# Optimization experiments

Hardware: AMD Instinct MI355X
Metric: run time of the kernel (lower is better)

The kernel has to match this reference:

```python
import jax, jax.numpy as jnp
import numpy as np

B, N, D = 8, 1024, 512
H = 8
DH = D // H
EPS_DIST = 1e-8
EPS_LN = 1e-5


def _layer_norm(x, gamma, beta):
    mu = jnp.mean(x, axis=-1, keepdims=True)
    var = jnp.mean((x - mu) ** 2, axis=-1, keepdims=True)
    return (x - mu) * jax.lax.rsqrt(var + EPS_LN) * gamma + beta


def setup_inputs() -> dict:
    key = jax.random.key(0)
    ks = jax.random.split(key, 6)
    scale = 1.0 / np.sqrt(D)
    inp = {
        "x": jax.random.normal(ks[0], (B, N, D), dtype=jnp.float32),
        "Wq": jax.random.normal(ks[1], (D, D), dtype=jnp.float32) * scale,
        "Wk": jax.random.normal(ks[2], (D, D), dtype=jnp.float32) * scale,
        "Wv": jax.random.normal(ks[3], (D, D), dtype=jnp.float32) * scale,
        "Wo": jax.random.normal(ks[4], (D, D), dtype=jnp.float32) * scale,
        "bq": jnp.zeros((D,), jnp.float32),
        "bk": jnp.zeros((D,), jnp.float32),
        "bv": jnp.zeros((D,), jnp.float32),
        "bo": jnp.zeros((D,), jnp.float32),
        "ln1_g": jnp.ones((D,), jnp.float32),
        "ln1_b": jnp.zeros((D,), jnp.float32),
        "ln2_g": jnp.ones((D,), jnp.float32),
        "ln2_b": jnp.zeros((D,), jnp.float32),
    }
    return inp


def reference(x, Wq, bq, Wk, bk, Wv, bv, Wo, bo, ln1_g, ln1_b, ln2_g, ln2_b):
    residual = x
    h = _layer_norm(x, ln1_g, ln1_b)  # pre-norm

    def heads(t):
        # [B,N,D] -> [B,H,N,DH]
        return t.reshape(B, N, H, DH).transpose(0, 2, 1, 3)

    q = heads(h @ Wq + bq)
    k = heads(h @ Wk + bk)
    v = heads(h @ Wv + bv)

    # Euclidean pairwise distance via ||q||^2 + ||k||^2 - 2 q.k expansion
    q_sq = jnp.sum(q * q, axis=-1)[..., :, None]      # [B,H,N,1]
    k_sq = jnp.sum(k * k, axis=-1)[..., None, :]      # [B,H,1,N]
    qk = jnp.einsum("bhnd,bhmd->bhnm", q, k)          # [B,H,N,N]
    d2 = jnp.maximum(q_sq + k_sq - 2.0 * qk, 0.0)
    dist = jnp.sqrt(d2 + EPS_DIST)

    # distance -> attention score: smaller distance = higher attention
    attn = jax.nn.softmax(-dist, axis=-1)             # [B,H,N,N]

    out = jnp.einsum("bhnm,bhmd->bhnd", attn, v)      # [B,H,N,DH]
    out = out.transpose(0, 2, 1, 3).reshape(B, N, D)
    out = out @ Wo + bo

    y = residual + out
    y = _layer_norm(y, ln2_g, ln2_b)
    return y
```

## Files before the change

kernel.cpp:

```cpp
#include <hip/hip_runtime.h>
#include <math.h>

typedef __attribute__((ext_vector_type(8))) short short8;
typedef __attribute__((ext_vector_type(4))) float f32x4;
typedef __attribute__((ext_vector_type(2))) unsigned uint2v;

constexpr int B  = 8;
constexpr int N  = 1024;
constexpr int D  = 512;
constexpr int H  = 8;
constexpr int DH = 64;
constexpr int M_ROWS = 8192;
constexpr float EPS_DIST = 1e-8f;
constexpr float EPS_LN   = 1e-5f;

__device__ inline unsigned short bfbits(float f) {
    union { float f; unsigned u; } v; v.f = f;
    unsigned r = v.u + 0x7fffu + ((v.u >> 16) & 1u);
    return (unsigned short)(r >> 16);
}
__device__ inline float bf2f(unsigned short s) {
    union { unsigned u; float f; } v; v.u = ((unsigned)s) << 16; return v.f;
}

__device__ inline void async_ld16(unsigned short* lds, const unsigned short* g) {
    __builtin_amdgcn_global_load_lds(
        (const __attribute__((address_space(1))) unsigned int*)(g),
        (__attribute__((address_space(3))) unsigned int*)(lds),
        16, 0, 0);
}

__global__ __launch_bounds__(256) void prep_kernel(const float* __restrict__ Wq,
                                                   const float* __restrict__ Wk,
                                                   const float* __restrict__ Wv,
                                                   const float* __restrict__ Wo,
                                                   unsigned short* __restrict__ WtAll,
                                                   const float* __restrict__ x,
                                                   const float* __restrict__ ln1_g,
                                                   const float* __restrict__ ln1_b,
                                                   unsigned short* __restrict__ h_bf) {
    const int bxg = blockIdx.x;
    if (bxg < 256) {
        int sub = bxg >> 6;
        const float* W = sub == 0 ? Wq : sub == 1 ? Wk : sub == 2 ? Wv : Wo;
        unsigned short* Wt = WtAll + (size_t)sub * 262144;
        int t = (bxg & 63) * 256 + threadIdx.x;
        int tn = t & 127, tk = t >> 7;
        int k = tk * 4, n = tn * 4;
        float4 r0 = *(const float4*)&W[(size_t)(k + 0) * 512 + n];
        float4 r1 = *(const float4*)&W[(size_t)(k + 1) * 512 + n];
        float4 r2 = *(const float4*)&W[(size_t)(k + 2) * 512 + n];
        float4 r3 = *(const float4*)&W[(size_t)(k + 3) * 512 + n];
        ushort4 c;
        c.x = bfbits(r0.x); c.y = bfbits(r1.x); c.z = bfbits(r2.x); c.w = bfbits(r3.x);
        *(ushort4*)&Wt[(size_t)(n + 0) * 512 + k] = c;
        c.x = bfbits(r0.y); c.y = bfbits(r1.y); c.z = bfbits(r2.y); c.w = bfbits(r3.y);
        *(ushort4*)&Wt[(size_t)(n + 1) * 512 + k] = c;
        c.x = bfbits(r0.z); c.y = bfbits(r1.z); c.z = bfbits(r2.z); c.w = bfbits(r3.z);
        *(ushort4*)&Wt[(size_t)(n + 2) * 512 + k] = c;
        c.x = bfbits(r0.w); c.y = bfbits(r1.w); c.z = bfbits(r2.w); c.w = bfbits(r3.w);
        *(ushort4*)&Wt[(size_t)(n + 3) * 512 + k] = c;
    } else {
        const int w = threadIdx.x >> 6, lane = threadIdx.x & 63;
        const int row = (bxg - 256) * 4 + w;
        const float4* xr = (const float4*)(x + (size_t)row * D);
        float4 a = xr[lane], b2 = xr[lane + 64];
        float s = a.x + a.y + a.z + a.w + b2.x + b2.y + b2.z + b2.w;
        #pragma unroll
        for (int o = 1; o < 64; o <<= 1) s += __shfl_xor(s, o, 64);
        const float mu = s * (1.0f / 512.0f);
        float d0 = a.x - mu, d1 = a.y - mu, d2 = a.z - mu, d3 = a.w - mu;
        float e0 = b2.x - mu, e1 = b2.y - mu, e2 = b2.z - mu, e3 = b2.w - mu;
        float vs = d0*d0 + d1*d1 + d2*d2 + d3*d3 + e0*e0 + e1*e1 + e2*e2 + e3*e3;
        #pragma unroll
        for (int o = 1; o < 64; o <<= 1) vs += __shfl_xor(vs, o, 64);
        const float rstd = rsqrtf(vs * (1.0f / 512.0f) + EPS_LN);
        const float4* g4 = (const float4*)ln1_g;
        const float4* b4 = (const float4*)ln1_b;
        float4 ga = g4[lane], gb = g4[lane + 64];
        float4 ba = b4[lane], bb = b4[lane + 64];
        ushort4 u;
        u.x = bfbits(d0 * rstd * ga.x + ba.x);
        u.y = bfbits(d1 * rstd * ga.y + ba.y);
        u.z = bfbits(d2 * rstd * ga.z + ba.z);
        u.w = bfbits(d3 * rstd * ga.w + ba.w);
        *(ushort4*)&h_bf[(size_t)row * 512 + lane * 4] = u;
        u.x = bfbits(e0 * rstd * gb.x + bb.x);
        u.y = bfbits(e1 * rstd * gb.y + bb.y);
        u.z = bfbits(e2 * rstd * gb.z + bb.z);
        u.w = bfbits(e3 * rstd * gb.w + bb.w);
        *(ushort4*)&h_bf[(size_t)row * 512 + 256 + lane * 4] = u;
    }
}

__global__ __launch_bounds__(256) void ln2_kernel(const unsigned short* __restrict__ y0,
                                                  const float* __restrict__ res,
                                                  const float* __restrict__ gamma,
                                                  const float* __restrict__ beta,
                                                  float* __restrict__ out) {
    const int w = threadIdx.x >> 6, lane = threadIdx.x & 63;
    const int row = blockIdx.x * 4 + w;
    const ushort4* y4 = (const ushort4*)(y0 + (size_t)row * D);
    const float4*  r4 = (const float4*)(res + (size_t)row * D);
    ushort4 ya = y4[lane], yb = y4[lane + 64];
    float4  ra = r4[lane], rb = r4[lane + 64];
    float v0 = bf2f(ya.x) + ra.x, v1 = bf2f(ya.y) + ra.y;
    float v2 = bf2f(ya.z) + ra.z, v3 = bf2f(ya.w) + ra.w;
    float v4 = bf2f(yb.x) + rb.x, v5 = bf2f(yb.y) + rb.y;
    float v6 = bf2f(yb.z) + rb.z, v7 = bf2f(yb.w) + rb.w;
    float s = v0 + v1 + v2 + v3 + v4 + v5 + v6 + v7;
    #pragma unroll
    for (int o = 1; o < 64; o <<= 1) s += __shfl_xor(s, o, 64);
    const float mu = s * (1.0f / 512.0f);
    v0 -= mu; v1 -= mu; v2 -= mu; v3 -= mu;
    v4 -= mu; v5 -= mu; v6 -= mu; v7 -= mu;
    float vs = v0*v0 + v1*v1 + v2*v2 + v3*v3 + v4*v4 + v5*v5 + v6*v6 + v7*v7;
    #pragma unroll
    for (int o = 1; o < 64; o <<= 1) vs += __shfl_xor(vs, o, 64);
    const float rstd = rsqrtf(vs * (1.0f / 512.0f) + EPS_LN);
    const float4* g4 = (const float4*)gamma;
    const float4* b4 = (const float4*)beta;
    float4 ga = g4[lane], gb = g4[lane + 64];
    float4 ba = b4[lane], bb = b4[lane + 64];
    float4 o1, o2;
    o1.x = v0 * rstd * ga.x + ba.x; o1.y = v1 * rstd * ga.y + ba.y;
    o1.z = v2 * rstd * ga.z + ba.z; o1.w = v3 * rstd * ga.w + ba.w;
    o2.x = v4 * rstd * gb.x + bb.x; o2.y = v5 * rstd * gb.y + bb.y;
    o2.z = v6 * rstd * gb.z + bb.z; o2.w = v7 * rstd * gb.w + bb.w;
    float4* orow = (float4*)(out + (size_t)row * D);
    orow[lane]      = o1;
    orow[lane + 64] = o2;
}

template <int MODE, int MT>
__global__ __launch_bounds__(256) void gemm128(const unsigned short* __restrict__ A,
                                               const unsigned short* __restrict__ Wt,
                                               const float* __restrict__ bias0,
                                               const float* __restrict__ bias1,
                                               const float* __restrict__ bias2,
                                               void* __restrict__ o0,
                                               unsigned short* __restrict__ Ko,
                                               unsigned short* __restrict__ Vo,
                                               float* __restrict__ sq0,
                                               float* __restrict__ sq1) {
    constexpr int RB = M_ROWS / MT;
    constexpr int NI = MT / 32;
    constexpr int ASZ = MT * 64, BSZ = 128 * 64;
    constexpr int SMSZ = (MODE == 1) ? ((ASZ + BSZ > 18432) ? ASZ + BSZ : 18432)
                                     : (ASZ + BSZ);
    __shared__ unsigned short smem[SMSZ];
    unsigned short* As = smem;
    unsigned short* Bs = smem + ASZ;

    const int id = blockIdx.x;
    const int by = id & (RB - 1), bx = id / RB;
    const int tid = threadIdx.x;
    const int lane = tid & 63, wv = tid >> 6;
    const int quad = lane >> 4, l15 = lane & 15;
    const int row0 = by * MT, col0 = bx * 128;
    const int wm = (wv & 1) * (MT / 2), wn = (wv >> 1) * 64;

    f32x4 acc[NI][4];
    #pragma unroll
    for (int i = 0; i < NI; ++i)
        #pragma unroll
        for (int j = 0; j < 4; ++j) acc[i][j] = (f32x4){0.f, 0.f, 0.f, 0.f};

    const unsigned short* Ag = A  + (size_t)row0 * 512;
    const unsigned short* Bg = Wt + (size_t)col0 * 512;

    for (int k0 = 0; k0 < 512; k0 += 64) {
        __syncthreads();
        #pragma unroll
        for (int c = 0; c < ASZ / 2048; ++c) {
            int fu = c * 2048 + tid * 8;
            int r = fu >> 6, ko = fu & 63;
            async_ld16(As + fu, Ag + (size_t)r * 512 + k0 + ko);
        }
        #pragma unroll
        for (int c = 0; c < BSZ / 2048; ++c) {
            int fu = c * 2048 + tid * 8;
            int r = fu >> 6, ko = fu & 63;
            async_ld16(Bs + fu, Bg + (size_t)r * 512 + k0 + ko);
        }
        __syncthreads();

        #pragma unroll
        for (int ks = 0; ks < 2; ++ks) {
            short8 af[NI], bf[4];
            #pragma unroll
            for (int i = 0; i < NI; ++i)
                af[i] = *(const short8*)&As[(wm + i * 16 + l15) * 64 + ks * 32 + quad * 8];
            #pragma unroll
            for (int j = 0; j < 4; ++j)
                bf[j] = *(const short8*)&Bs[(wn + j * 16 + l15) * 64 + ks * 32 + quad * 8];
            #pragma unroll
            for (int i = 0; i < NI; ++i)
                #pragma unroll
                for (int j = 0; j < 4; ++j)
                    acc[i][j] = __builtin_amdgcn_mfma_f32_16x16x32_bf16(af[i], bf[j], acc[i][j], 0, 0, 0);
        }
    }

    if (MODE == 0) {
        unsigned short* C = (unsigned short*)o0;
        #pragma unroll
        for (int i = 0; i < NI; ++i)
            #pragma unroll
            for (int j = 0; j < 4; ++j) {
                int col = col0 + wn + j * 16 + l15;
                float bv = bias0[col];
                #pragma unroll
                for (int r = 0; r < 4; ++r) {
                    int row = row0 + wm + i * 16 + quad * 4 + r;
                    C[(size_t)row * 512 + col] = bfbits(acc[i][j][r] + bv);
                }
            }
    } else {
        const int colg = col0 + wn;
        const int seg = colg >> 9;
        const int hh = (colg & 511) >> 6;
        const float* bias = seg == 0 ? bias0 : seg == 1 ? bias1 : bias2;

        if (seg < 2) {
            unsigned short* dst = seg == 0 ? (unsigned short*)o0 : Ko;
            float* sq = seg == 0 ? sq0 : sq1;
            #pragma unroll
            for (int i = 0; i < NI; ++i) {
                const int m0 = row0 + wm + i * 16 + quad * 4;
                float ss[4] = {0.f, 0.f, 0.f, 0.f};
                #pragma unroll
                for (int j = 0; j < 4; ++j) {
                    float bvj = bias[hh * 64 + j * 16 + l15];
                    #pragma unroll
                    for (int r = 0; r < 4; ++r) {
                        float v = acc[i][j][r] + bvj;
                        unsigned short ub = bfbits(v);
                        float vr = bf2f(ub);
                        ss[r] += vr * vr;
                        int m = m0 + r;
                        int b_ = m >> 10, n_ = m & 1023;
                        dst[((size_t)((b_ * 8 + hh) * 1024) + n_) * 64 + j * 16 + l15] = ub;
                    }
                }
                #pragma unroll
                for (int r = 0; r < 4; ++r) {
                    float s = ss[r];
                    s += __shfl_xor(s, 1, 64);
                    s += __shfl_xor(s, 2, 64);
                    s += __shfl_xor(s, 4, 64);
                    s += __shfl_xor(s, 8, 64);
                    if (l15 == 0) {
                        int m = m0 + r;
                        sq[(size_t)((m >> 10) * 8 + hh) * 1024 + (m & 1023)] = s;
                    }
                }
            }
        } else {
            __syncthreads();
            unsigned short* T = smem + wv * 4608;
            #pragma unroll
            for (int i = 0; i < NI; ++i)
                #pragma unroll
                for (int j = 0; j < 4; ++j) {
                    float bvj = bias[hh * 64 + j * 16 + l15];
                    ushort4 pk;
                    pk.x = bfbits(acc[i][j][0] + bvj);
                    pk.y = bfbits(acc[i][j][1] + bvj);
                    pk.z = bfbits(acc[i][j][2] + bvj);
                    pk.w = bfbits(acc[i][j][3] + bvj);
                    *(ushort4*)&T[(j * 16 + l15) * 72 + i * 16 + quad * 4] = pk;
                }
            const int b_ = (row0 + wm) >> 10;
            const int nbase = (row0 + wm) & 1023;
            unsigned short* Vg = Vo + ((size_t)((b_ * 8 + hh) * 64)) * 1024 + nbase;
            #pragma unroll
            for (int it = 0; it < 8; ++it) {
                int dl = it * 8 + (lane >> 3);
                int nl = (lane & 7) * 8;
                uint4 v = *(const uint4*)&T[dl * 72 + nl];
                *(uint4*)&Vg[(size_t)dl * 1024 + nl] = v;
            }
        }
    }
}

__global__ __launch_bounds__(256) void attn_kernel(const unsigned short* __restrict__ Q,
                                                   const unsigned short* __restrict__ K,
                                                   const unsigned short* __restrict__ Vt,
                                                   const float* __restrict__ qsq,
                                                   const float* __restrict__ ksq,
                                                   unsigned short* __restrict__ O) {
    __shared__ unsigned short Ks[2][64][64];
    __shared__ unsigned short Vs[2][64][64];
    __shared__ float ksq_s[2][64];

    const int id = blockIdx.x;
    const int bh = id & 63, qb = id >> 6;
    const int q0 = qb * 128;
    const int tid = threadIdx.x;
    const int lane = tid & 63, w = tid >> 6;
    const int quad = lane >> 4, l15 = lane & 15;
    const int b_ = bh >> 3, h_ = bh & 7;

    const unsigned short* Qb = Q  + (size_t)bh * N * DH;
    const unsigned short* Kb = K  + (size_t)bh * N * DH;
    const unsigned short* Vb = Vt + (size_t)bh * DH * N;

    short8 qf[2][2];
    #pragma unroll
    for (int qh = 0; qh < 2; ++qh) {
        const unsigned short* qp = Qb + (size_t)(q0 + w * 32 + qh * 16 + l15) * 64 + quad * 8;
        qf[qh][0] = *(const short8*)qp;
        qf[qh][1] = *(const short8*)(qp + 32);
        unsigned* qw = (unsigned*)&qf[qh][0];
        #pragma unroll
        for (int j = 0; j < 8; ++j) qw[j] = (qw[j] ^ 0x80008000u) + 0x00800080u;
    }
    float qe[2];
    qe[0] = qsq[bh * N + q0 + w * 32 + l15] + EPS_DIST;
    qe[1] = qsq[bh * N + q0 + w * 32 + 16 + l15] + EPS_DIST;

    f32x4 oacc[2][4];
    #pragma unroll
    for (int qh = 0; qh < 2; ++qh)
        #pragma unroll
        for (int dt = 0; dt < 4; ++dt) oacc[qh][dt] = (f32x4){0.f, 0.f, 0.f, 0.f};
    float dsum[2] = {0.f, 0.f};

    const int r0s = tid >> 3, r1s = r0s + 32;
    const int cbase = (tid & 7) * 8;
    const int csw = cbase ^ ((r0s & 7) << 3);
    uint4 kreg0, kreg1, vreg0, vreg1;
    float ksreg = 0.f;

    kreg0 = *(const uint4*)(Kb + (size_t)r0s * 64 + cbase);
    kreg1 = *(const uint4*)(Kb + (size_t)r1s * 64 + cbase);
    vreg0 = *(const uint4*)(Vb + (size_t)r0s * N + cbase);
    vreg1 = *(const uint4*)(Vb + (size_t)r1s * N + cbase);
    if (tid < 64) ksreg = ksq[bh * N + tid];

    *(uint4*)&Ks[0][r0s][csw] = kreg0;
    *(uint4*)&Ks[0][r1s][csw] = kreg1;
    *(uint4*)&Vs[0][r0s][csw] = vreg0;
    *(uint4*)&Vs[0][r1s][csw] = vreg1;
    if (tid < 64) ksq_s[0][tid] = ksreg;
    __syncthreads();

    for (int kt = 0; kt < 16; ++kt) {
        const int cur = kt & 1;
        if (kt < 15) {
            kreg0 = *(const uint4*)(Kb + (size_t)((kt + 1) * 64 + r0s) * 64 + cbase);
            kreg1 = *(const uint4*)(Kb + (size_t)((kt + 1) * 64 + r1s) * 64 + cbase);
            vreg0 = *(const uint4*)(Vb + (size_t)r0s * N + (kt + 1) * 64 + cbase);
            vreg1 = *(const uint4*)(Vb + (size_t)r1s * N + (kt + 1) * 64 + cbase);
            if (tid < 64) ksreg = ksq[bh * N + (kt + 1) * 64 + tid];
        }

        #pragma unroll
        for (int kc = 0; kc < 2; ++kc) {
            unsigned Wp[2][2][2];
            #pragma unroll
            for (int kh = 0; kh < 2; ++kh) {
                const int kb = kc * 2 + kh;
                const int krow = kb * 16 + l15;
                const int ksw = (krow & 7) << 3;
                short8 kf0 = *(const short8*)&Ks[cur][krow][(quad * 8) ^ ksw];
                short8 kf1 = *(const short8*)&Ks[cur][krow][(32 + quad * 8) ^ ksw];
                f32x4 ks2 = *(const f32x4*)&ksq_s[cur][kb * 16 + quad * 4];
                #pragma unroll
                for (int qh = 0; qh < 2; ++qh) {
                    f32x4 sa;
                    #pragma unroll
                    for (int r = 0; r < 4; ++r) sa[r] = ks2[r] + qe[qh];
                    sa = __builtin_amdgcn_mfma_f32_16x16x32_bf16(kf0, qf[qh][0], sa, 0, 0, 0);
                    sa = __builtin_amdgcn_mfma_f32_16x16x32_bf16(kf1, qf[qh][1], sa, 0, 0, 0);
                    float pr[4];
                    #pragma unroll
                    for (int r = 0; r < 4; ++r) {
                        float d2 = fmaxf(sa[r], EPS_DIST);
                        float p = __expf(-__builtin_amdgcn_sqrtf(d2));
                        dsum[qh] += p;
                        pr[r] = p;
                    }
                    union { float f; unsigned u; } u0, u1, u2, u3;
                    u0.f = pr[0]; u1.f = pr[1]; u2.f = pr[2]; u3.f = pr[3];
                    Wp[qh][kh][0] = (u1.u & 0xFFFF0000u) | (u0.u >> 16);
                    Wp[qh][kh][1] = (u3.u & 0xFFFF0000u) | (u2.u >> 16);
                }
            }

            short8 vf[4];
            #pragma unroll
            for (int dt = 0; dt < 4; ++dt) {
                const int vrow = dt * 16 + l15;
                vf[dt] = *(const short8*)&Vs[cur][vrow][(kc * 32 + quad * 8) ^ ((vrow & 7) << 3)];
            }

            #pragma unroll
            for (int qh = 0; qh < 2; ++qh) {
                uint2v ya = __builtin_amdgcn_permlane32_swap(Wp[qh][0][0], Wp[qh][1][0], false, false);
                uint2v za = __builtin_amdgcn_permlane16_swap(ya.x, ya.y, false, false);
                uint2v yb = __builtin_amdgcn_permlane32_swap(Wp[qh][0][1], Wp[qh][1][1], false, false);
                uint2v zb = __builtin_amdgcn_permlane16_swap(yb.x, yb.y, false, false);
                union { unsigned wds[4]; short8 s; } pu;
                pu.wds[0] = za.x; pu.wds[1] = zb.x; pu.wds[2] = za.y; pu.wds[3] = zb.y;
                short8 pf = pu.s;
                #pragma unroll
                for (int dt = 0; dt < 4; ++dt)
                    oacc[qh][dt] = __builtin_amdgcn_mfma_f32_16x16x32_bf16(pf, vf[dt], oacc[qh][dt], 0, 0, 0);
            }
        }

        if (kt < 15) {
            *(uint4*)&Ks[cur ^ 1][r0s][csw] = kreg0;
            *(uint4*)&Ks[cur ^ 1][r1s][csw] = kreg1;
            *(uint4*)&Vs[cur ^ 1][r0s][csw] = vreg0;
            *(uint4*)&Vs[cur ^ 1][r1s][csw] = vreg1;
            if (tid < 64) ksq_s[cur ^ 1][tid] = ksreg;
        }
        __syncthreads();
    }

    float rinv[2];
    #pragma unroll
    for (int qh = 0; qh < 2; ++qh) {
        float s = dsum[qh];
        s += __shfl_xor(s, 16, 64);
        s += __shfl_xor(s, 32, 64);
        rinv[qh] = __builtin_amdgcn_rcpf(s);
    }

    float* sc = (float*)ksq_s;
    if (lane < 16) {
        sc[w * 32 + l15]      = rinv[0];
        sc[w * 32 + 16 + l15] = rinv[1];
    }
    f32x4 rv[2];
    rv[0] = *(const f32x4*)&sc[w * 32 + quad * 4];
    rv[1] = *(const f32x4*)&sc[w * 32 + 16 + quad * 4];

    #pragma unroll
    for (int qh = 0; qh < 2; ++qh)
        #pragma unroll
        for (int dt = 0; dt < 4; ++dt)
            #pragma unroll
            for (int r = 0; r < 4; ++r) {
                int n_ = q0 + w * 32 + qh * 16 + quad * 4 + r;
                O[((size_t)(b_ * N + n_) * D) + h_ * DH + dt * 16 + l15] =
                    bfbits(oacc[qh][dt][r] * rv[qh][r]);
            }
}

extern "C" void kernel_launch(void* const* d_in, const int* in_sizes, int n_in,
                              void* d_out, int out_size, void* d_ws, size_t ws_size,
                              hipStream_t stream) {
    const float* x     = (const float*)d_in[0];
    const float* Wq    = (const float*)d_in[1];
    const float* Wk    = (const float*)d_in[2];
    const float* Wv    = (const float*)d_in[3];
    const float* Wo    = (const float*)d_in[4];
    const float* bq    = (const float*)d_in[5];
    const float* bk    = (const float*)d_in[6];
    const float* bv    = (const float*)d_in[7];
    const float* bo    = (const float*)d_in[8];
    const float* ln1_g = (const float*)d_in[9];
    const float* ln1_b = (const float*)d_in[10];
    const float* ln2_g = (const float*)d_in[11];
    const float* ln2_b = (const float*)d_in[12];
    float* out = (float*)d_out;

    unsigned short* WtAll = (unsigned short*)d_ws;
    unsigned short* h_bf  = WtAll + 4 * 262144;
    unsigned short* Qb    = h_bf + 4194304;
    unsigned short* Kb    = Qb + 4194304;
    unsigned short* Vtg   = Kb + 4194304;
    unsigned short* Ob    = Vtg + 4194304;
    unsigned short* Y0    = Ob + 4194304;
    float* qsq = (float*)(Y0 + 4194304);
    float* ksq = qsq + 65536;

    prep_kernel<<<256 + M_ROWS / 4, 256, 0, stream>>>(Wq, Wk, Wv, Wo, WtAll,
                                                      x, ln1_g, ln1_b, h_bf);

    gemm128<1, 128><<<768, 256, 0, stream>>>(h_bf, WtAll, bq, bk, bv,
                                             Qb, Kb, Vtg, qsq, ksq);

    attn_kernel<<<512, 256, 0, stream>>>(Qb, Kb, Vtg, qsq, ksq, Ob);

    gemm128<0, 64><<<512, 256, 0, stream>>>(Ob, WtAll + 3 * 262144, bo,
                                            nullptr, nullptr, Y0,
                                            nullptr, nullptr, nullptr, nullptr);

    ln2_kernel<<<M_ROWS / 4, 256, 0, stream>>>(Y0, x, ln2_g, ln2_b, out);
}
```

Baseline: 180.8 us.

## Double attention query tile per block and compute softmax row sums via MFMA

Each attention block now handles 256 queries instead of 128, with each wave owning 64 query rows, so every K/V tile loaded into shared memory is reused across twice as many queries and the grid halves to 256 blocks. The row sums of the softmax numerators are accumulated with an extra MFMA against a ones vector rather than scalar adds, which removes the cross-lane shuffle and shared-memory reduction at the end. The bf16 packing uses a byte-permute instruction. In exchange, register pressure rises (launch bounds set to 1 block), only 256 blocks fill the GPU, and the row sums are now taken over bf16-rounded probabilities.

```diff
diff --git a/kernel.cpp b/kernel.cpp
--- a/kernel.cpp
+++ b/kernel.cpp
@@ -285,19 +285,19 @@
     }
 }
 
-__global__ __launch_bounds__(256) void attn_kernel(const unsigned short* __restrict__ Q,
-                                                   const unsigned short* __restrict__ K,
-                                                   const unsigned short* __restrict__ Vt,
-                                                   const float* __restrict__ qsq,
-                                                   const float* __restrict__ ksq,
-                                                   unsigned short* __restrict__ O) {
+__global__ __launch_bounds__(256, 1) void attn_kernel(const unsigned short* __restrict__ Q,
+                                                      const unsigned short* __restrict__ K,
+                                                      const unsigned short* __restrict__ Vt,
+                                                      const float* __restrict__ qsq,
+                                                      const float* __restrict__ ksq,
+                                                      unsigned short* __restrict__ O) {
     __shared__ unsigned short Ks[2][64][64];
     __shared__ unsigned short Vs[2][64][64];
     __shared__ float ksq_s[2][64];
 
     const int id = blockIdx.x;
     const int bh = id & 63, qb = id >> 6;
-    const int q0 = qb * 128;
+    const int q0 = qb * 256;
     const int tid = threadIdx.x;
     const int lane = tid & 63, w = tid >> 6;
     const int quad = lane >> 4, l15 = lane & 15;
@@ -307,26 +307,31 @@
     const unsigned short* Kb = K  + (size_t)bh * N * DH;
     const unsigned short* Vb = Vt + (size_t)bh * DH * N;
 
-    short8 qf[2][2];
-    #pragma unroll
-    for (int qh = 0; qh < 2; ++qh) {
-        const unsigned short* qp = Qb + (size_t)(q0 + w * 32 + qh * 16 + l15) * 64 + quad * 8;
+    short8 qf[4][2];
+    #pragma unroll
+    for (int qh = 0; qh < 4; ++qh) {
+        const unsigned short* qp = Qb + (size_t)(q0 + w * 64 + qh * 16 + l15) * 64 + quad * 8;
         qf[qh][0] = *(const short8*)qp;
         qf[qh][1] = *(const short8*)(qp + 32);
         unsigned* qw = (unsigned*)&qf[qh][0];
         #pragma unroll
         for (int j = 0; j < 8; ++j) qw[j] = (qw[j] ^ 0x80008000u) + 0x00800080u;
     }
-    float qe[2];
-    qe[0] = qsq[bh * N + q0 + w * 32 + l15] + EPS_DIST;
-    qe[1] = qsq[bh * N + q0 + w * 32 + 16 + l15] + EPS_DIST;
-
-    f32x4 oacc[2][4];
-    #pragma unroll
-    for (int qh = 0; qh < 2; ++qh)
+    float qe[4];
+    #pragma unroll
+    for (int qh = 0; qh < 4; ++qh)
+        qe[qh] = qsq[bh * N + q0 + w * 64 + qh * 16 + l15] + EPS_DIST;
+
+    const short8 onesf = {0x3F80, 0x3F80, 0x3F80, 0x3F80, 0x3F80, 0x3F80, 0x3F80, 0x3F80};
+
+    f32x4 oacc[4][4];
+    f32x4 dsum[4];
+    #pragma unroll
+    for (int qh = 0; qh < 4; ++qh) {
+        dsum[qh] = (f32x4){0.f, 0.f, 0.f, 0.f};
         #pragma unroll
         for (int dt = 0; dt < 4; ++dt) oacc[qh][dt] = (f32x4){0.f, 0.f, 0.f, 0.f};
-    float dsum[2] = {0.f, 0.f};
+    }
 
     const int r0s = tid >> 3, r1s = r0s + 32;
     const int cbase = (tid & 7) * 8;
@@ -359,7 +364,7 @@
 
         #pragma unroll
         for (int kc = 0; kc < 2; ++kc) {
-            unsigned Wp[2][2][2];
+            unsigned Wp[4][2][2];
             #pragma unroll
             for (int kh = 0; kh < 2; ++kh) {
                 const int kb = kc * 2 + kh;
@@ -369,7 +374,7 @@
                 short8 kf1 = *(const short8*)&Ks[cur][krow][(32 + quad * 8) ^ ksw];
                 f32x4 ks2 = *(const f32x4*)&ksq_s[cur][kb * 16 + quad * 4];
                 #pragma unroll
-                for (int qh = 0; qh < 2; ++qh) {
+                for (int qh = 0; qh < 4; ++qh) {
                     f32x4 sa;
                     #pragma unroll
                     for (int r = 0; r < 4; ++r) sa[r] = ks2[r] + qe[qh];
@@ -379,14 +384,12 @@
                     #pragma unroll
                     for (int r = 0; r < 4; ++r) {
                         float d2 = fmaxf(sa[r], EPS_DIST);
-                        float p = __expf(-__builtin_amdgcn_sqrtf(d2));
-                        dsum[qh] += p;
-                        pr[r] = p;
+                        pr[r] = __expf(-__builtin_amdgcn_sqrtf(d2));
                     }
                     union { float f; unsigned u; } u0, u1, u2, u3;
                     u0.f = pr[0]; u1.f = pr[1]; u2.f = pr[2]; u3.f = pr[3];
-                    Wp[qh][kh][0] = (u1.u & 0xFFFF0000u) | (u0.u >> 16);
-                    Wp[qh][kh][1] = (u3.u & 0xFFFF0000u) | (u2.u >> 16);
+                    Wp[qh][kh][0] = __builtin_amdgcn_perm(u1.u, u0.u, 0x07060302u);
+                    Wp[qh][kh][1] = __builtin_amdgcn_perm(u3.u, u2.u, 0x07060302u);
                 }
             }
 
@@ -398,7 +401,7 @@
             }
 
             #pragma unroll
-            for (int qh = 0; qh < 2; ++qh) {
+            for (int qh = 0; qh < 4; ++qh) {
                 uint2v ya = __builtin_amdgcn_permlane32_swap(Wp[qh][0][0], Wp[qh][1][0], false, false);
                 uint2v za = __builtin_amdgcn_permlane16_swap(ya.x, ya.y, false, false);
                 uint2v yb = __builtin_amdgcn_permlane32_swap(Wp[qh][0][1], Wp[qh][1][1], false, false);
@@ -406,6 +409,7 @@
                 union { unsigned wds[4]; short8 s; } pu;
                 pu.wds[0] = za.x; pu.wds[1] = zb.x; pu.wds[2] = za.y; pu.wds[3] = zb.y;
                 short8 pf = pu.s;
+                dsum[qh] = __builtin_amdgcn_mfma_f32_16x16x32_bf16(pf, onesf, dsum[qh], 0, 0, 0);
                 #pragma unroll
                 for (int dt = 0; dt < 4; ++dt)
                     oacc[qh][dt] = __builtin_amdgcn_mfma_f32_16x16x32_bf16(pf, vf[dt], oacc[qh][dt], 0, 0, 0);
@@ -422,34 +426,20 @@
         __syncthreads();
     }
 
-    float rinv[2];
-    #pragma unroll
-    for (int qh = 0; qh < 2; ++qh) {
-        float s = dsum[qh];
-        s += __shfl_xor(s, 16, 64);
-        s += __shfl_xor(s, 32, 64);
-        rinv[qh] = __builtin_amdgcn_rcpf(s);
-    }
-
-    float* sc = (float*)ksq_s;
-    if (lane < 16) {
-        sc[w * 32 + l15]      = rinv[0];
-        sc[w * 32 + 16 + l15] = rinv[1];
-    }
-    f32x4 rv[2];
-    rv[0] = *(const f32x4*)&sc[w * 32 + quad * 4];
-    rv[1] = *(const f32x4*)&sc[w * 32 + 16 + quad * 4];
-
-    #pragma unroll
-    for (int qh = 0; qh < 2; ++qh)
+    #pragma unroll
+    for (int qh = 0; qh < 4; ++qh) {
+        f32x4 rv;
+        #pragma unroll
+        for (int r = 0; r < 4; ++r) rv[r] = __builtin_amdgcn_rcpf(dsum[qh][r]);
         #pragma unroll
         for (int dt = 0; dt < 4; ++dt)
             #pragma unroll
             for (int r = 0; r < 4; ++r) {
-                int n_ = q0 + w * 32 + qh * 16 + quad * 4 + r;
+                int n_ = q0 + w * 64 + qh * 16 + quad * 4 + r;
                 O[((size_t)(b_ * N + n_) * D) + h_ * DH + dt * 16 + l15] =
-                    bfbits(oacc[qh][dt][r] * rv[qh][r]);
-            }
+                    bfbits(oacc[qh][dt][r] * rv[r]);
+            }
+    }
 }
 
 extern "C" void kernel_launch(void* const* d_in, const int* in_sizes, int n_in,
@@ -486,7 +476,7 @@
     gemm128<1, 128><<<768, 256, 0, stream>>>(h_bf, WtAll, bq, bk, bv,
                                              Qb, Kb, Vtg, qsq, ksq);
 
-    attn_kernel<<<512, 256, 0, stream>>>(Qb, Kb, Vtg, qsq, ksq, Ob);
+    attn_kernel<<<256, 256, 0, stream>>>(Qb, Kb, Vtg, qsq, ksq, Ob);
 
     gemm128<0, 64><<<512, 256, 0, stream>>>(Ob, WtAll + 3 * 262144, bo,
                                             nullptr, nullptr, Y0,
```

Result: no change. 181.2 us (+0.2%).
